# Optimization experiments

Hardware: AMD Instinct MI355X
Metric: run time of the kernel (lower is better)

The kernel has to match this reference:

```python
import jax, jax.numpy as jnp
import numpy as np

NUM_BEAM, NUM_NULL, NUM_BIN, NUM_CH = 8, 4, 257, 8
NUM_BLOCK, NUM_FRAME = 8, 500
ALPHA, LOW_FREQ, HIGH_FREQ = 0.35, 5, 70


def setup_inputs() -> dict:
    key = jax.random.key(0)
    k1, k2, k3, k4 = jax.random.split(key, 4)
    return {
        "input": jax.random.normal(k1, (NUM_BLOCK, NUM_FRAME, 2, NUM_BIN, NUM_CH), jnp.float32),
        "beam_id": jax.random.randint(k2, (NUM_BLOCK,), 0, NUM_BEAM),
        "targ_w": jax.random.normal(k3, (NUM_BEAM, 2, NUM_BIN, NUM_CH), jnp.float32),
        "null_w": jax.random.normal(k4, (NUM_BEAM, NUM_NULL, 2, NUM_BIN, NUM_CH), jnp.float32),
    }


def _forward(input, beam_id, targ_w, null_w):
    a = ALPHA
    xr, xi = input[:, :, 0], input[:, :, 1]            # (B,T,F,C)
    # target beamformer: select per-block complex weights (B,2,F,C)
    tw = targ_w[beam_id]
    twr, twi = tw[:, 0], tw[:, 1]                      # (B,F,C)
    tr = jnp.einsum('btfc,bfc->btf', xr, twr) - jnp.einsum('btfc,bfc->btf', xi, twi)
    ti = jnp.einsum('btfc,bfc->btf', xr, twi) + jnp.einsum('btfc,bfc->btf', xi, twr)
    tr, ti = tr[..., None], ti[..., None]              # (B,T,F,1)
    # null beamformer: (B,N,2,F,C)
    nw = null_w[beam_id]
    nwr, nwi = nw[:, :, 0], nw[:, :, 1]                # (B,N,F,C)
    nr = jnp.einsum('btfc,bnfc->btfn', xr, nwr) - jnp.einsum('btfc,bnfc->btfn', xi, nwi)
    ni = jnp.einsum('btfc,bnfc->btfn', xr, nwi) + jnp.einsum('btfc,bnfc->btfn', xi, nwr)
    # elementwise cross-spectra products (B,T,F,N)
    pr = tr * nr + ti * ni
    pi = ti * nr - tr * ni
    pw = jnp.mean(xr ** 2 + xi ** 2, axis=-1, keepdims=True)  # (B,T,F,1)

    # t = 0 (note: (1-alpha) scales only the FIRST product, as in the source)
    phi_r0 = (1.0 - a) * tr[:, 0] * nr[:, 0] + ti[:, 0] * ni[:, 0]
    phi_i0 = (1.0 - a) * ti[:, 0] * nr[:, 0] - tr[:, 0] * ni[:, 0]
    psd0 = (1.0 - a) * pw[:, 0]
    phi0 = jnp.sqrt(phi_r0 ** 2 + phi_i0 ** 2)
    dcf0 = jnp.clip(phi0 / (psd0 + 1e-13), 0.01, 1.0)

    def step(carry, xs):
        phi_r, phi_i, psd = carry
        pr_t, pi_t, pw_t = xs
        phi_r = a * phi_r + (1.0 - a) * pr_t
        phi_i = a * phi_i + (1.0 - a) * pi_t
        psd = a * psd + (1.0 - a) * pw_t
        phi = jnp.sqrt(phi_r ** 2 + phi_i ** 2)
        dcf_t = jnp.clip(phi / (psd + 1e-13), 0.01, 1.0)
        pre = jnp.sum(psd[:, LOW_FREQ:HIGH_FREQ, :], axis=1, keepdims=True)
        aft = jnp.sum(phi[:, LOW_FREQ:HIGH_FREQ, :], axis=1, keepdims=True)
        ratio = jnp.clip(aft / (pre + 1e-10), 0.01, 1.0)
        dcf_t = jnp.sqrt(dcf_t * ratio)
        return (phi_r, phi_i, psd), dcf_t

    xs = (jnp.moveaxis(pr[:, 1:], 1, 0),
          jnp.moveaxis(pi[:, 1:], 1, 0),
          jnp.moveaxis(pw[:, 1:], 1, 0))
    _, dcf_rest = jax.lax.scan(step, (phi_r0, phi_i0, psd0), xs)  # (T-1,B,F,N)
    dcf = jnp.concatenate([dcf0[None], dcf_rest], axis=0)
    dcf = jnp.moveaxis(dcf, 0, 1)                                 # (B,T,F,N)
    targ_out = jnp.stack([tr[..., 0], ti[..., 0]], axis=2)        # (B,T,2,F)
    return dcf, targ_out


def reference(input, beam_id, targ_w, null_w):
    return _forward(input, beam_id, targ_w, null_w)
```

## Files before the change

kernel.cpp:

```cpp
#include <hip/hip_runtime.h>

#define NB 8
#define NT 500
#define NF 257
#define NC 8
#define NNUL 4
#define LOWF 5
#define HIGHF 70
#define S_CHUNK 8
#define WARM 4
#define N_CHUNK 63
#define AL 0.35f

__device__ __forceinline__ float dot4(const float4& a, const float4& b) {
    return a.x*b.x + a.y*b.y + a.z*b.z + a.w*b.w;
}
__device__ __forceinline__ float dot8(const float4& a0, const float4& a1,
                                      const float4& b0, const float4& b1) {
    return dot4(a0, b0) + dot4(a1, b1);
}
__device__ __forceinline__ float fast_rcp(float v) {
#if __has_builtin(__builtin_amdgcn_rcpf)
    return __builtin_amdgcn_rcpf(v);
#else
    return 1.0f / v;
#endif
}
__device__ __forceinline__ float fast_sqrt(float v) {
#if __has_builtin(__builtin_amdgcn_sqrtf)
    return __builtin_amdgcn_sqrtf(v);
#else
    return sqrtf(v);
#endif
}
__device__ __forceinline__ float clamp01(float v) {
#if __has_builtin(__builtin_amdgcn_fmed3f)
    return __builtin_amdgcn_fmed3f(v, 0.01f, 1.0f);
#else
    return fminf(fmaxf(v, 0.01f), 1.0f);
#endif
}

__global__ __launch_bounds__(1024, 4) void dcf_fused_kernel(
    const float* __restrict__ x,
    const int* __restrict__ beam_id,
    const float* __restrict__ targ_w,
    const float* __restrict__ null_w,
    float* __restrict__ out)
{
    const int tid = threadIdx.x;
    const int bid = blockIdx.x;
    const int b  = bid & 7;
    const int k  = bid >> 3;
    const int t0 = k * S_CHUNK;
    const int te = min(NT, t0 + S_CHUNK);
    int ts = t0 - WARM; if (ts < 0) ts = 0;

    const int f = tid >> 2;
    const int n = tid & 3;
    const int wid = tid >> 6;
    const int lane = tid & 63;
    const bool extra = (tid >= 1020);

    __shared__ float s_w256[16 + 4 * 16];
    __shared__ float s_part[S_CHUNK][25];
    __shared__ float s_dcf[S_CHUNK][1028];

    const int beam = beam_id[b];
    const int pA = n & 1;
    const int offA = pA * (NF * NC);
    const int offB = (1 - pA) * (NF * NC);
    const int psel = (n == 1 || n == 2) ? 1 : 0;
    const float nsign = pA ? -1.f : 1.f;

    float4 tw0, tw1, w10, w11, w20, w21, w30, w31, w40, w41;
    {
        const float* tp = targ_w + ((size_t)(beam * 2 + psel) * NF + f) * NC;
        tw0 = *(const float4*)(tp);  tw1 = *(const float4*)(tp + 4);
        const float* qp  = null_w + ((size_t)((beam * NNUL + n) * 2) * NF + f) * NC;
        const float* qpx = null_w + ((size_t)((beam * NNUL + (n ^ 1)) * 2) * NF + f) * NC;
        w10 = *(const float4*)(qp  + offA);  w11 = *(const float4*)(qp  + offA + 4);
        w20 = *(const float4*)(qp  + offB);  w21 = *(const float4*)(qp  + offB + 4);
        w30 = *(const float4*)(qpx + offA);  w31 = *(const float4*)(qpx + offA + 4);
        w40 = *(const float4*)(qpx + offB);  w41 = *(const float4*)(qpx + offB + 4);
    }
    if (tid < 16) {
        int p = tid >> 3, c = tid & 7;
        s_w256[tid] = targ_w[((size_t)(beam * 2 + p) * NF + 256) * NC + c];
    } else if (tid < 80) {
        int i = tid - 16;
        int nn = i >> 4, p = (i >> 3) & 1, c = i & 7;
        s_w256[tid] = null_w[((size_t)((beam * NNUL + nn) * 2 + p) * NF + 256) * NC + c];
    }
    __syncthreads();

    float phi_r = 0.f, phi_i = 0.f, psd = 0.f;
    float phi_r2 = 0.f, phi_i2 = 0.f, psd2 = 0.f;
    const float a = AL, oma = 1.0f - AL;
    const int rl = 2 * NF * NC;
    const bool in_red = (f >= LOWF) && (f < HIGHF);

    const float* xpa = x + (size_t)(b * NT + ts) * rl + f * NC + offA;
    float4 pA0 = *(const float4*)(xpa);
    float4 pA1 = *(const float4*)(xpa + 4);

    float* outT = out + (size_t)NB * NT * NF * NNUL;
    float* poT = outT + ((size_t)(b * NT + t0) * 2 + n) * NF + f;
    float* sdp = &s_dcf[0][tid];
    float* spp = &s_part[0][wid * 5];

    for (int t = ts; t < te; ++t) {
        const float4 A0 = pA0, A1 = pA1;
        xpa += rl;
        if (t + 1 < te) {
            pA0 = *(const float4*)(xpa);
            pA1 = *(const float4*)(xpa + 4);
        }

        const float d = dot8(A0, A1, tw0, tw1);
        const float e = __shfl_xor(d, 1);
        const float u = (n < 2) ? ((n == 0) ? (d - e) : (e - d)) : (d + e);
        const float v = __shfl_xor(u, 2);
        const float tr = (n < 2) ? u : v;
        const float ti = (n < 2) ? v : u;

        const float P  = dot8(A0, A1, w10, w11);
        const float X  = dot8(A0, A1, w20, w21);
        const float s3 = dot8(A0, A1, w30, w31);
        const float s4 = dot8(A0, A1, w40, w41);
        const float Q  = __shfl_xor(s3, 1);
        const float Y  = __shfl_xor(s4, 1);
        const float nr = nsign * (P - Q);
        const float ni = X + Y;

        float sq = dot4(A0, A0) + dot4(A1, A1);
        sq += __shfl_xor(sq, 1);
        const float pw = sq * 0.125f;

        if (t == 0) {
            phi_r = oma * tr * nr + ti * ni;
            phi_i = oma * ti * nr - tr * ni;
            psd   = oma * pw;
        } else {
            phi_r = a * phi_r + oma * (tr * nr + ti * ni);
            phi_i = a * phi_i + oma * (ti * nr - tr * ni);
            psd   = a * psd + oma * pw;
        }

        float tr2 = 0.f, ti2 = 0.f;
        if (extra) {
            const float* xe = xpa + (NC - rl);
            const float4 eA0 = *(const float4*)(xe);
            const float4 eA1 = *(const float4*)(xe + 4);
            const float4 etw0 = *(const float4*)&s_w256[psel * 8];
            const float4 etw1 = *(const float4*)&s_w256[psel * 8 + 4];
            const float* nq  = &s_w256[16 + n * 16];
            const float* nqx = &s_w256[16 + (n ^ 1) * 16];
            const float4 e10 = *(const float4*)(nq  + pA * 8);
            const float4 e11 = *(const float4*)(nq  + pA * 8 + 4);
            const float4 e20 = *(const float4*)(nq  + (1 - pA) * 8);
            const float4 e21 = *(const float4*)(nq  + (1 - pA) * 8 + 4);
            const float4 e30 = *(const float4*)(nqx + pA * 8);
            const float4 e31 = *(const float4*)(nqx + pA * 8 + 4);
            const float4 e40 = *(const float4*)(nqx + (1 - pA) * 8);
            const float4 e41 = *(const float4*)(nqx + (1 - pA) * 8 + 4);
            const float d2 = dot8(eA0, eA1, etw0, etw1);
            const float e2 = __shfl_xor(d2, 1);
            const float u2 = (n < 2) ? ((n == 0) ? (d2 - e2) : (e2 - d2)) : (d2 + e2);
            const float v2 = __shfl_xor(u2, 2);
            tr2 = (n < 2) ? u2 : v2;
            ti2 = (n < 2) ? v2 : u2;
            const float P2  = dot8(eA0, eA1, e10, e11);
            const float X2  = dot8(eA0, eA1, e20, e21);
            const float s32 = dot8(eA0, eA1, e30, e31);
            const float s42 = dot8(eA0, eA1, e40, e41);
            const float Q2  = __shfl_xor(s32, 1);
            const float Y2  = __shfl_xor(s42, 1);
            const float nr2 = nsign * (P2 - Q2);
            const float ni2 = X2 + Y2;
            float sq2 = dot4(eA0, eA0) + dot4(eA1, eA1);
            sq2 += __shfl_xor(sq2, 1);
            const float pw2 = sq2 * 0.125f;
            if (t == 0) {
                phi_r2 = oma * tr2 * nr2 + ti2 * ni2;
                phi_i2 = oma * ti2 * nr2 - tr2 * ni2;
                psd2   = oma * pw2;
            } else {
                phi_r2 = a * phi_r2 + oma * (tr2 * nr2 + ti2 * ni2);
                phi_i2 = a * phi_i2 + oma * (ti2 * nr2 - tr2 * ni2);
                psd2   = a * psd2 + oma * pw2;
            }
        }

        if (t >= t0) {
            const float phi = fast_sqrt(phi_r * phi_r + phi_i * phi_i);
            const float dcfv = clamp01(phi * fast_rcp(psd + 1e-13f));
            if (n < 2) *poT = (n == 0) ? tr : ti;
            *sdp = dcfv;
            if (extra) {
                const float phi2 = fast_sqrt(phi_r2 * phi_r2 + phi_i2 * phi_i2);
                const float dcf2v = clamp01(phi2 * fast_rcp(psd2 + 1e-13f));
                sdp[4] = dcf2v;
                if (n < 2) poT[1] = (n == 0) ? tr2 : ti2;
            }
            if (wid < 5) {
                float v_phi = in_red ? phi : 0.f;
                float v_psd = (in_red && n == 0) ? psd : 0.f;
                #pragma unroll
                for (int off = 4; off < 64; off <<= 1) {
                    v_phi += __shfl_xor(v_phi, off);
                    v_psd += __shfl_xor(v_psd, off);
                }
                if (lane < 4)  spp[lane] = v_phi;
                if (lane == 0) spp[4]    = v_psd;
            }
            poT += 2 * NF; sdp += 1028; spp += 25;
        }
    }

    __syncthreads();

    float* po = out + ((size_t)(b * NT + t0) * NF + f) * NNUL + n;
    const float* sdr = &s_dcf[0][tid];
    const float* spr = &s_part[0][0];
    const int nf = te - t0;
    for (int fr = 0; fr < nf; ++fr) {
        const int t = t0 + fr;
        float dcfv = sdr[0];
        float dcf2v = extra ? sdr[4] : 0.f;
        if (t >= 1) {
            const float pre = spr[4] + spr[9] + spr[14] + spr[19] + spr[24];
            const float aft = spr[n] + spr[5 + n] + spr[10 + n] + spr[15 + n] + spr[20 + n];
            const float ratio = clamp01(aft * fast_rcp(pre + 1e-10f));
            dcfv = fast_sqrt(dcfv * ratio);
            if (extra) dcf2v = fast_sqrt(dcf2v * ratio);
        }
        *po = dcfv;
        if (extra) po[NNUL] = dcf2v;
        po += NF * NNUL; sdr += 1028; spr += 25;
    }
}

extern "C" void kernel_launch(void* const* d_in, const int* in_sizes, int n_in,
                              void* d_out, int out_size, void* d_ws, size_t ws_size,
                              hipStream_t stream) {
    const float* x       = (const float*)d_in[0];
    const int*   beam_id = (const int*)d_in[1];
    const float* targ_w  = (const float*)d_in[2];
    const float* null_w  = (const float*)d_in[3];
    float* out           = (float*)d_out;
    (void)d_ws; (void)ws_size;

    dcf_fused_kernel<<<dim3(NB * N_CHUNK), dim3(1024), 0, stream>>>(
        x, beam_id, targ_w, null_w, out);
}
```

Before: 129.7 us.

## Move band reduction out of time loop and stage bin-256 inputs in LDS

```diff
diff --git a/kernel.cpp b/kernel.cpp
--- a/kernel.cpp
+++ b/kernel.cpp
@@ -63,7 +63,9 @@
     const bool extra = (tid >= 1020);
 
     __shared__ float s_w256[16 + 4 * 16];
+    __shared__ float s_xe[12 * 16];
     __shared__ float s_part[S_CHUNK][25];
+    __shared__ float s_psd[S_CHUNK][260];
     __shared__ float s_dcf[S_CHUNK][1028];
 
     const int beam = beam_id[b];
@@ -72,6 +74,7 @@
     const int offB = (1 - pA) * (NF * NC);
     const int psel = (n == 1 || n == 2) ? 1 : 0;
     const float nsign = pA ? -1.f : 1.f;
+    const int rl = 2 * NF * NC;
 
     float4 tw0, tw1, w10, w11, w20, w21, w30, w31, w40, w41;
     {
@@ -91,14 +94,21 @@
         int i = tid - 16;
         int nn = i >> 4, p = (i >> 3) & 1, c = i & 7;
         s_w256[tid] = null_w[((size_t)((beam * NNUL + nn) * 2 + p) * NF + 256) * NC + c];
+    } else if (tid >= 128 && tid < 176) {
+        const int i = tid - 128;
+        const int c = i >> 1, h = i & 1;
+        const int fr = c >> 1, p = c & 1;
+        if (fr < te - ts) {
+            const float* src = x + (size_t)(b * NT + ts + fr) * rl
+                             + p * (NF * NC) + 256 * NC + h * 4;
+            *(float4*)&s_xe[fr * 16 + p * 8 + h * 4] = *(const float4*)src;
+        }
     }
     __syncthreads();
 
     float phi_r = 0.f, phi_i = 0.f, psd = 0.f;
     float phi_r2 = 0.f, phi_i2 = 0.f, psd2 = 0.f;
     const float a = AL, oma = 1.0f - AL;
-    const int rl = 2 * NF * NC;
-    const bool in_red = (f >= LOWF) && (f < HIGHF);
 
     const float* xpa = x + (size_t)(b * NT + ts) * rl + f * NC + offA;
     float4 pA0 = *(const float4*)(xpa);
@@ -107,7 +117,7 @@
     float* outT = out + (size_t)NB * NT * NF * NNUL;
     float* poT = outT + ((size_t)(b * NT + t0) * 2 + n) * NF + f;
     float* sdp = &s_dcf[0][tid];
-    float* spp = &s_part[0][wid * 5];
+    float* spq = &s_psd[0][f];
 
     for (int t = ts; t < te; ++t) {
         const float4 A0 = pA0, A1 = pA1;
@@ -149,7 +159,7 @@
 
         float tr2 = 0.f, ti2 = 0.f;
         if (extra) {
-            const float* xe = xpa + (NC - rl);
+            const float* xe = &s_xe[(t - ts) * 16 + pA * 8];
             const float4 eA0 = *(const float4*)(xe);
             const float4 eA1 = *(const float4*)(xe + 4);
             const float4 etw0 = *(const float4*)&s_w256[psel * 8];
@@ -194,28 +204,39 @@
 
         if (t >= t0) {
             const float phi = fast_sqrt(phi_r * phi_r + phi_i * phi_i);
-            const float dcfv = clamp01(phi * fast_rcp(psd + 1e-13f));
             if (n < 2) *poT = (n == 0) ? tr : ti;
-            *sdp = dcfv;
+            *sdp = phi;
+            if (n == 0) *spq = psd;
             if (extra) {
                 const float phi2 = fast_sqrt(phi_r2 * phi_r2 + phi_i2 * phi_i2);
-                const float dcf2v = clamp01(phi2 * fast_rcp(psd2 + 1e-13f));
-                sdp[4] = dcf2v;
+                sdp[4] = phi2;
+                if (n == 0) spq[1] = psd2;
                 if (n < 2) poT[1] = (n == 0) ? tr2 : ti2;
             }
-            if (wid < 5) {
-                float v_phi = in_red ? phi : 0.f;
-                float v_psd = (in_red && n == 0) ? psd : 0.f;
-                #pragma unroll
-                for (int off = 4; off < 64; off <<= 1) {
-                    v_phi += __shfl_xor(v_phi, off);
-                    v_psd += __shfl_xor(v_psd, off);
-                }
-                if (lane < 4)  spp[lane] = v_phi;
-                if (lane == 0) spp[4]    = v_psd;
-            }
-            poT += 2 * NF; sdp += 1028; spp += 25;
-        }
+            poT += 2 * NF; sdp += 1028; spq += 260;
+        }
+    }
+
+    __syncthreads();
+
+    const int nf = te - t0;
+    if (wid < 8 && wid < nf && (t0 + wid) >= 1) {
+        const int fr = wid;
+        const float* sd = &s_dcf[fr][0];
+        float vp = sd[20 + lane] + sd[84 + lane] + sd[148 + lane] + sd[212 + lane];
+        if (lane < 4) vp += sd[276 + lane];
+        const float* sp2 = &s_psd[fr][0];
+        float vq = sp2[5 + lane];
+        if (lane == 0) vq += sp2[69];
+        vq += __shfl_xor(vq, 1);
+        vq += __shfl_xor(vq, 2);
+        #pragma unroll
+        for (int off = 4; off < 64; off <<= 1) {
+            vp += __shfl_xor(vp, off);
+            vq += __shfl_xor(vq, off);
+        }
+        if (lane < 4)  s_part[fr][lane] = vp;
+        if (lane == 0) s_part[fr][4]    = vq;
     }
 
     __syncthreads();
@@ -223,21 +244,22 @@
     float* po = out + ((size_t)(b * NT + t0) * NF + f) * NNUL + n;
     const float* sdr = &s_dcf[0][tid];
     const float* spr = &s_part[0][0];
-    const int nf = te - t0;
+    const float* sqr = &s_psd[0][f];
     for (int fr = 0; fr < nf; ++fr) {
         const int t = t0 + fr;
-        float dcfv = sdr[0];
-        float dcf2v = extra ? sdr[4] : 0.f;
+        float dcfv = clamp01(sdr[0] * fast_rcp(sqr[0] + 1e-13f));
+        float dcf2v = 0.f;
+        if (extra) dcf2v = clamp01(sdr[4] * fast_rcp(sqr[1] + 1e-13f));
         if (t >= 1) {
-            const float pre = spr[4] + spr[9] + spr[14] + spr[19] + spr[24];
-            const float aft = spr[n] + spr[5 + n] + spr[10 + n] + spr[15 + n] + spr[20 + n];
+            const float pre = spr[4];
+            const float aft = spr[n];
             const float ratio = clamp01(aft * fast_rcp(pre + 1e-10f));
             dcfv = fast_sqrt(dcfv * ratio);
             if (extra) dcf2v = fast_sqrt(dcf2v * ratio);
         }
         *po = dcfv;
         if (extra) po[NNUL] = dcf2v;
-        po += NF * NNUL; sdr += 1028; spr += 25;
+        po += NF * NNUL; sdr += 1028; spr += 25; sqr += 260;
     }
 }
 
```

After: 127.0 us. 1.02x faster.
